# Kernel optimization log

Measured on AMD Instinct MI355X. Metric: run time of the kernel, lower is better.

Reference implementation:

```python
import jax, jax.numpy as jnp
import numpy as np


def _tridiag_solve(x, d, l, u):
    # Build dense tridiagonal M (faithful to the torch module) and solve.
    # x: [B, N, F]; d: [F]; l, u: [F-1]
    diag = jax.nn.softplus(d) + 2.0
    M = jnp.diag(diag) + jnp.diag(jnp.tanh(l), -1) + jnp.diag(jnp.tanh(u), 1)
    # solve M @ Y = x^T  -> Y: [B, F, N], then transpose back
    y = jnp.linalg.solve(M, jnp.swapaxes(x, -2, -1))
    return jnp.swapaxes(y, -2, -1)


def setup_inputs() -> dict:
    key = jax.random.key(0)
    ks = jax.random.split(key, 11)
    B, N = 8, 4096
    IN, HID, OUT = 512, 2048, 512
    s = 0.02
    return {
        "x": jax.random.normal(ks[0], (B, N, IN), dtype=jnp.float32),
        "d1": jax.random.normal(ks[1], (IN,), dtype=jnp.float32) * s,
        "l1": jax.random.normal(ks[2], (IN - 1,), dtype=jnp.float32) * s,
        "u1": jax.random.normal(ks[3], (IN - 1,), dtype=jnp.float32) * s,
        "W1": jax.random.normal(ks[4], (HID, IN), dtype=jnp.float32) * s,
        "b1": jax.random.normal(ks[5], (HID,), dtype=jnp.float32) * s,
        "d2": jax.random.normal(ks[6], (HID,), dtype=jnp.float32) * s,
        "l2": jax.random.normal(ks[7], (HID - 1,), dtype=jnp.float32) * s,
        "u2": jax.random.normal(ks[8], (HID - 1,), dtype=jnp.float32) * s,
        "W2": jax.random.normal(ks[9], (OUT, HID), dtype=jnp.float32) * s,
        "b2": jax.random.normal(ks[10], (OUT,), dtype=jnp.float32) * s,
    }


def reference(x, d1, l1, u1, W1, b1, d2, l2, u2, W2, b2):
    h = _tridiag_solve(x, d1, l1, u1)
    h = jax.nn.relu(jnp.einsum("bnf,hf->bnh", h, W1) + b1)
    h = _tridiag_solve(h, d2, l2, u2)
    out = jnp.einsum("bnh,oh->bno", h, W2) + b2
    return out
```

## Files before the change

### kernel.cpp

```cpp
#include <hip/hip_runtime.h>
#include <cstdint>

#define R_ROWS 32768
#define F1 512
#define F2 2048
#define NOUT 512

typedef __bf16 bf16x8 __attribute__((ext_vector_type(8)));
typedef float f32x4 __attribute__((ext_vector_type(4)));

__device__ __forceinline__ float bf2f(uint16_t b) {
  union { uint32_t u; float f; } v; v.u = ((uint32_t)b) << 16; return v.f;
}
__device__ __forceinline__ uint16_t f2bf(float f) {
  union { float f; uint32_t u; } v; v.f = f;
  uint32_t u = v.u;
  return (uint16_t)((u + 0x7fffu + ((u >> 16) & 1u)) >> 16);
}

union U4 { uint4 v; uint16_t s[8]; };

__global__ void sniff_kernel(const uint16_t* x, int* flag) {
  if (threadIdx.x == 0) {
    int bad = 0;
    for (int i = 0; i < 64; ++i) {
      uint32_t e = (x[i] >> 7) & 0xFFu;
      if (e != 0u && (e < 90u || e > 141u)) bad++;
    }
    *flag = (bad >= 8) ? 1 : 0;
  }
}

__global__ void conv_xb(const float* x, const float* b1, const float* b2,
                        uint16_t* xb, uint16_t* b1b, uint16_t* b2b,
                        const int* flag) {
  if (*flag != 1) return;
  const int NX = R_ROWS * F1 / 4;
  int q = blockIdx.x * blockDim.x + threadIdx.x;
  const float* src; uint16_t* dst; int base;
  if (q < NX)                        { src = x;  dst = xb;  base = q; }
  else if (q < NX + F2 / 4)          { src = b1; dst = b1b; base = q - NX; }
  else if (q < NX + F2/4 + NOUT/4)   { src = b2; dst = b2b; base = q - NX - F2/4; }
  else return;
  float4 v = ((const float4*)src)[base];
  ushort4 o;
  o.x = f2bf(v.x); o.y = f2bf(v.y); o.z = f2bf(v.z); o.w = f2bf(v.w);
  ((ushort4*)dst)[base] = o;
}

__launch_bounds__(256)
__global__ void prep_fused(const void* d1, const void* l1, const void* u1,
                           const void* d2, const void* l2, const void* u2,
                           float* f1, float* f2, const int* flag) {
  const bool inf32 = (*flag == 1);
  const int F = blockIdx.x ? F2 : F1;
  float* base = blockIdx.x ? f2 : f1;
  const void* dp = blockIdx.x ? d2 : d1;
  const void* lp = blockIdx.x ? l2 : l1;
  const void* up = blockIdx.x ? u2 : u1;

  __shared__ float sdiag[F2], stl[F2], stu[F2];

  for (int i = threadIdx.x; i < F; i += 256) {
    float dv = inf32 ? ((const float*)dp)[i] : bf2f(((const uint16_t*)dp)[i]);
    sdiag[i] = log1pf(expf(dv)) + 2.0f;
    bool in = i < F - 1;
    float lv = in ? (inf32 ? ((const float*)lp)[i] : bf2f(((const uint16_t*)lp)[i])) : 0.0f;
    float uv = in ? (inf32 ? ((const float*)up)[i] : bf2f(((const uint16_t*)up)[i])) : 0.0f;
    stl[i] = in ? tanhf(lv) : 0.0f;
    stu[i] = in ? tanhf(uv) : 0.0f;
  }
  __syncthreads();

  const int t  = threadIdx.x;
  const int CH = F >> 8;
  const int s0 = t * CH;
  const int j0 = (s0 >= 16) ? (s0 - 16) : 0;
  float b  = sdiag[j0];
  float ib = __builtin_amdgcn_rcpf(b);
  for (int j = j0 + 1; j < s0; ++j) {
    b  = fmaf(-stu[j - 1] * stl[j - 1], ib, sdiag[j]);
    ib = __builtin_amdgcn_rcpf(b);
  }
  #pragma unroll
  for (int q = 0; q < 8; ++q) {
    if (q >= CH) break;
    int i = s0 + q;
    float w, nb;
    if (i == 0) { w = 0.0f; nb = sdiag[0]; }
    else        { w = stu[i - 1] * ib; nb = fmaf(-w, stl[i - 1], sdiag[i]); }
    ib = __builtin_amdgcn_rcpf(nb);
    base[3 * F + i] = w;
    base[4 * F + i] = ib;
    base[5 * F + i] = stl[i] * ib;
  }
}

template<int F>
__launch_bounds__(256)
__global__ void solve_fused(const void* X, uint16_t* Y, const float* fact,
                            const int* flag, int allow_f32) {
  const bool inf32 = allow_f32 && (*flag == 1);
  constexpr int LPR = F / 32;
  constexpr int FP = F + (F >> 5);
  __shared__ float sfw[FP], sib[FP], sbk[FP];
  __shared__ uint4 sout[1024];
  for (int i = threadIdx.x; i < F; i += 256) {
    int ii = i + (i >> 5);
    sfw[ii] = fact[3 * F + i];
    sib[ii] = fact[4 * F + i];
    sbk[ii] = fact[5 * F + i];
  }
  __syncthreads();
  const int tid = threadIdx.x;
  int gt  = blockIdx.x * 256 + tid;
  int row = gt / LPR;
  int j   = gt % LPR;
  int k0  = j * 32;
  const size_t rb = (size_t)row * F;

  float xc[32];
  if (inf32) {
    const float* xr = (const float*)X + rb + k0;
    #pragma unroll
    for (int t = 0; t < 8; ++t) {
      float4 v = ((const float4*)xr)[t];
      xc[4*t] = v.x; xc[4*t+1] = v.y; xc[4*t+2] = v.z; xc[4*t+3] = v.w;
    }
  } else {
    const uint16_t* xr = (const uint16_t*)X + rb + k0;
    #pragma unroll
    for (int t = 0; t < 4; ++t) {
      U4 in; in.v = ((const uint4*)xr)[t];
      #pragma unroll
      for (int s = 0; s < 8; ++s) xc[8*t+s] = bf2f(in.s[s]);
    }
  }

  float dp = 0.0f;
  if (j > 0) {
    float xw[16];
    if (inf32) {
      const float* xr = (const float*)X + rb + k0 - 16;
      #pragma unroll
      for (int t = 0; t < 4; ++t) {
        float4 v = ((const float4*)xr)[t];
        xw[4*t] = v.x; xw[4*t+1] = v.y; xw[4*t+2] = v.z; xw[4*t+3] = v.w;
      }
    } else {
      const uint16_t* xr = (const uint16_t*)X + rb + k0 - 16;
      #pragma unroll
      for (int t = 0; t < 2; ++t) {
        U4 in; in.v = ((const uint4*)xr)[t];
        #pragma unroll
        for (int s = 0; s < 8; ++s) xw[8*t+s] = bf2f(in.s[s]);
      }
    }
    #pragma unroll
    for (int t = 0; t < 16; ++t) {
      int k = k0 - 16 + t;
      dp = fmaf(-sfw[k + (k >> 5)], dp, xw[t]);
    }
  }
  float dpv[32];
  #pragma unroll
  for (int t = 0; t < 32; ++t) {
    int k = k0 + t;
    dp = fmaf(-sfw[k + (k >> 5)], dp, xc[t]);
    dpv[t] = dp;
  }

  float wdp[16];
  #pragma unroll
  for (int t = 0; t < 16; ++t) wdp[t] = __shfl_down(dpv[t], 1);
  float yn = 0.0f;
  if (j < LPR - 1) {
    #pragma unroll
    for (int t = 15; t >= 0; --t) {
      int k = k0 + 32 + t;
      int kk = k + (k >> 5);
      yn = fmaf(-sbk[kk], yn, wdp[t] * sib[kk]);
    }
  }
  U4 out[4];
  #pragma unroll
  for (int t = 31; t >= 0; --t) {
    int k = k0 + t;
    int kk = k + (k >> 5);
    yn = fmaf(-sbk[kk], yn, dpv[t] * sib[kk]);
    out[t >> 3].s[t & 7] = f2bf(yn);
  }
  #pragma unroll
  for (int t = 0; t < 4; ++t) sout[tid * 4 + t] = out[t].v;
  __syncthreads();
  uint4* yg = (uint4*)Y + (size_t)blockIdx.x * 1024;
  #pragma unroll
  for (int i = 0; i < 4; ++i) yg[i * 256 + tid] = sout[i * 256 + tid];
}

__device__ __forceinline__ void gl_lds16(const uint16_t* g, uint16_t* l) {
  __builtin_amdgcn_global_load_lds((const __attribute__((address_space(1))) void*)g,
                                   (__attribute__((address_space(3))) void*)l, 16, 0, 0);
}

#define LOFF(bb, ab, h) ((bb) * 32768 + (ab) * 16384 + (h) * 8192)

#define GSTG(gp, bb, ab, h, kt) do {                                              \
    gl_lds16((gp) + (size_t)(h) * 128 * K + (kt),        lds + LOFF(bb, ab, h) + w * 512);        \
    gl_lds16((gp) + ((size_t)(h) * 128 + 64) * K + (kt), lds + LOFF(bb, ab, h) + 4096 + w * 512); \
  } while (0)

#define RD_A(mq) do {                                                             \
    _Pragma("unroll")                                                             \
    for (int fi = 0; fi < 4; ++fi) {                                              \
      af[fi][0] = *(const bf16x8*)(lds + curA + (mq) * 8192 + arow + fi * 1024 + c0); \
      af[fi][1] = *(const bf16x8*)(lds + curA + (mq) * 8192 + arow + fi * 1024 + c1); \
    }                                                                             \
  } while (0)

#define RD_B(nq) do {                                                             \
    _Pragma("unroll")                                                             \
    for (int fj = 0; fj < 2; ++fj) {                                              \
      bfr[nq][fj][0] = *(const bf16x8*)(lds + curB + (nq) * 8192 + brow + fj * 1024 + c0); \
      bfr[nq][fj][1] = *(const bf16x8*)(lds + curB + (nq) * 8192 + brow + fj * 1024 + c1); \
    }                                                                             \
  } while (0)

#define MMA_QUAD(mq, nq) do {                                                     \
    _Pragma("unroll")                                                             \
    for (int fi = 0; fi < 4; ++fi) {                                              \
      _Pragma("unroll")                                                           \
      for (int fj = 0; fj < 2; ++fj) {                                            \
        acc[(mq)*4+fi][(nq)*2+fj] = __builtin_amdgcn_mfma_f32_16x16x32_bf16(      \
            af[fi][0], bfr[nq][fj][0], acc[(mq)*4+fi][(nq)*2+fj], 0, 0, 0);       \
        acc[(mq)*4+fi][(nq)*2+fj] = __builtin_amdgcn_mfma_f32_16x16x32_bf16(      \
            af[fi][1], bfr[nq][fj][1], acc[(mq)*4+fi][(nq)*2+fj], 0, 0, 0);       \
      }                                                                           \
    }                                                                             \
  } while (0)

#define VMC(n) asm volatile("s_waitcnt vmcnt(" #n ")" ::: "memory")
#define BAR()  __builtin_amdgcn_s_barrier()
#define LGK0() do { asm volatile("s_waitcnt lgkmcnt(0)" ::: "memory");            \
                    __builtin_amdgcn_sched_barrier(0); } while (0)

template<bool RELU, bool FINAL, int NTN>
__launch_bounds__(512, 2)
__global__ void gemm8(const uint16_t* __restrict__ Aa, const uint16_t* __restrict__ Ab,
                      const uint16_t* __restrict__ Bw,
                      const uint16_t* __restrict__ bias0, const uint16_t* __restrict__ bias1,
                      void* __restrict__ Cout, int Nn, int K, const int* flag) {
  __shared__ __align__(16) uint16_t lds[65536];
  const int f = *flag;
  const uint16_t* A    = f ? Ab : Aa;
  const uint16_t* bias = f ? bias1 : bias0;

  const int tid = threadIdx.x;
  const int w = tid >> 6;
  const int l = tid & 63;
  const int wm = w >> 2;
  const int wn = w & 3;

  const int b = blockIdx.x;
  const int x = b & 7;
  const int g = b >> 3;
  const int nb = g & (NTN - 1);
  const int mb = (g / NTN) * 8 + x;
  const int MB = mb * 256, NB = nb * 256;
  const int NT = K >> 6;

  const int srow = w * 8 + (l >> 3);
  const int sch  = (l & 7) ^ ((l >> 3) & 7);
  const uint16_t* ag = A  + (size_t)(MB + srow) * K + sch * 8;
  const uint16_t* bg = Bw + (size_t)(NB + srow) * K + sch * 8;

  const int c0 = (((l >> 4) ^ (l & 7)) << 3);
  const int c1 = c0 ^ 32;
  const int arow = (wm * 64 + (l & 15)) * 64;
  const int brow = (wn * 32 + (l & 15)) * 64;

  f32x4 acc[8][4] = {};
  bf16x8 af[4][2];
  bf16x8 bfr[2][2][2];

  GSTG(ag, 0, 0, 0, 0);
  GSTG(bg, 0, 1, 0, 0);
  GSTG(bg, 0, 1, 1, 0);
  GSTG(ag, 0, 0, 1, 0);
  VMC(4);
  BAR();

  for (int t = 0; t < NT - 1; ++t) {
    const int cur  = t & 1;
    const int nxt  = cur ^ 1;
    const int curA = cur * 32768;
    const int curB = curA + 16384;
    const int kn   = (t + 1) * 64;
    RD_A(0); RD_B(0);
    GSTG(ag, nxt, 0, 0, kn);
    VMC(4); BAR(); LGK0();
    __builtin_amdgcn_s_setprio(1); MMA_QUAD(0, 0); __builtin_amdgcn_s_setprio(0);
    BAR();
    RD_B(1);
    GSTG(bg, nxt, 1, 0, kn);
    VMC(4); BAR(); LGK0();
    __builtin_amdgcn_s_setprio(1); MMA_QUAD(0, 1); __builtin_amdgcn_s_setprio(0);
    BAR();
    RD_A(1);
    GSTG(bg, nxt, 1, 1, kn);
    BAR(); LGK0();
    __builtin_amdgcn_s_setprio(1); MMA_QUAD(1, 0); __builtin_amdgcn_s_setprio(0);
    BAR();
    GSTG(ag, nxt, 0, 1, kn);
    VMC(4); BAR();
    __builtin_amdgcn_s_setprio(1); MMA_QUAD(1, 1); __builtin_amdgcn_s_setprio(0);
    BAR();
  }

  {
    const int curA = ((NT - 1) & 1) * 32768;
    const int curB = curA + 16384;
    RD_A(0); RD_B(0);
    __builtin_amdgcn_s_setprio(1); MMA_QUAD(0, 0); __builtin_amdgcn_s_setprio(0);
    VMC(2); BAR();
    RD_B(1);
    __builtin_amdgcn_s_setprio(1); MMA_QUAD(0, 1); __builtin_amdgcn_s_setprio(0);
    VMC(0); BAR();
    RD_A(1);
    MMA_QUAD(1, 0);
    MMA_QUAD(1, 1);
  }

  const bool outf32 = FINAL && (f != 0);
  const int ccol  = l & 15;
  const int crow4 = (l >> 4) * 4;
  #pragma unroll
  for (int j = 0; j < 4; ++j) {
    int gcol = NB + (j >> 1) * 128 + wn * 32 + (j & 1) * 16 + ccol;
    float bv = bf2f(bias[gcol]);
    #pragma unroll
    for (int i = 0; i < 8; ++i) {
      int grow = MB + (i >> 2) * 128 + wm * 64 + (i & 3) * 16 + crow4;
      #pragma unroll
      for (int rr = 0; rr < 4; ++rr) {
        float v = acc[i][j][rr] + bv;
        if (RELU) v = fmaxf(v, 0.0f);
        size_t idx = (size_t)(grow + rr) * Nn + gcol;
        if (outf32) ((float*)Cout)[idx]    = v;
        else        ((uint16_t*)Cout)[idx] = f2bf(v);
      }
    }
  }
}

extern "C" void kernel_launch(void* const* d_in, const int* in_sizes, int n_in,
                              void* d_out, int out_size, void* d_ws, size_t ws_size,
                              hipStream_t stream) {
  const void* x  = d_in[0];
  const void* d1 = d_in[1];
  const void* l1 = d_in[2];
  const void* u1 = d_in[3];
  const void* W1 = d_in[4];
  const void* b1 = d_in[5];
  const void* d2 = d_in[6];
  const void* l2 = d_in[7];
  const void* u2 = d_in[8];
  const void* W2 = d_in[9];
  const void* b2 = d_in[10];

  char* ws = (char*)d_ws;
  int*      flag = (int*)ws;
  float*    f1   = (float*)(ws + 256);
  float*    f2   = (float*)(ws + (64 << 10));
  uint16_t* b1b  = (uint16_t*)(ws + (128 << 10));
  uint16_t* b2b  = (uint16_t*)(ws + (136 << 10));
  uint16_t* W1s  = (uint16_t*)(ws + (1 << 20));
  uint16_t* W2s  = (uint16_t*)(ws + (3 << 20));
  uint16_t* xb   = (uint16_t*)(ws + ((size_t)8 << 20));
  uint16_t* H1   = (uint16_t*)(ws + ((size_t)40 << 20));

  sniff_kernel<<<1, 64, 0, stream>>>((const uint16_t*)x, flag);

  prep_fused<<<2, 256, 0, stream>>>(d1, l1, u1, d2, l2, u2, f1, f2, flag);

  solve_fused<F1><<<128, 256, 0, stream>>>(W1, W1s, f1, flag, 1);
  solve_fused<F2><<<128, 256, 0, stream>>>(W2, W2s, f2, flag, 1);

  {
    int quads = R_ROWS * F1 / 4 + F2 / 4 + NOUT / 4;
    conv_xb<<<(quads + 255) / 256, 256, 0, stream>>>(
        (const float*)x, (const float*)b1, (const float*)b2, xb, b1b, b2b, flag);
  }

  gemm8<true, false, 8><<<1024, 512, 0, stream>>>(
      (const uint16_t*)x, xb, W1s, (const uint16_t*)b1, b1b, H1, F2, F1, flag);

  gemm8<false, true, 2><<<256, 512, 0, stream>>>(
      H1, H1, W2s, (const uint16_t*)b2, b2b, d_out, NOUT, F2, flag);
}
```

Baseline: 319.2 us.

## Fuse preprocessing launches and cut barriers in the GEMM main loop

Folds the input-dtype sniff and bias conversion into the prep kernel. It also merges both weight tridiagonal solves and the x-to-bf16 conversion into one launch by splitting the work on block index. This removes three kernel launches and their serialization gaps. Separately, the GEMM main loop is rescheduled to issue more LDS fragment reads up front and wait on partial lgkmcnt counts, dropping from eight barriers per K-step to two. This raises register pressure and makes correctness depend on the hand-tuned waitcnt values.

```diff
diff --git a/kernel.cpp b/kernel.cpp
--- a/kernel.cpp
+++ b/kernel.cpp
@@ -20,39 +20,25 @@
 
 union U4 { uint4 v; uint16_t s[8]; };
 
-__global__ void sniff_kernel(const uint16_t* x, int* flag) {
-  if (threadIdx.x == 0) {
-    int bad = 0;
-    for (int i = 0; i < 64; ++i) {
-      uint32_t e = (x[i] >> 7) & 0xFFu;
-      if (e != 0u && (e < 90u || e > 141u)) bad++;
-    }
-    *flag = (bad >= 8) ? 1 : 0;
-  }
-}
-
-__global__ void conv_xb(const float* x, const float* b1, const float* b2,
-                        uint16_t* xb, uint16_t* b1b, uint16_t* b2b,
-                        const int* flag) {
-  if (*flag != 1) return;
-  const int NX = R_ROWS * F1 / 4;
-  int q = blockIdx.x * blockDim.x + threadIdx.x;
-  const float* src; uint16_t* dst; int base;
-  if (q < NX)                        { src = x;  dst = xb;  base = q; }
-  else if (q < NX + F2 / 4)          { src = b1; dst = b1b; base = q - NX; }
-  else if (q < NX + F2/4 + NOUT/4)   { src = b2; dst = b2b; base = q - NX - F2/4; }
-  else return;
-  float4 v = ((const float4*)src)[base];
-  ushort4 o;
-  o.x = f2bf(v.x); o.y = f2bf(v.y); o.z = f2bf(v.z); o.w = f2bf(v.w);
-  ((ushort4*)dst)[base] = o;
+__device__ __forceinline__ int sniff_x(const uint16_t* x) {
+  int bad = 0;
+  #pragma unroll 8
+  for (int i = 0; i < 64; ++i) {
+    uint32_t e = (x[i] >> 7) & 0xFFu;
+    if (e != 0u && (e < 90u || e > 141u)) bad++;
+  }
+  return (bad >= 8) ? 1 : 0;
 }
 
 __launch_bounds__(256)
-__global__ void prep_fused(const void* d1, const void* l1, const void* u1,
+__global__ void prep_fused(const void* x,
+                           const void* d1, const void* l1, const void* u1,
                            const void* d2, const void* l2, const void* u2,
-                           float* f1, float* f2, const int* flag) {
-  const bool inf32 = (*flag == 1);
+                           const void* b1, const void* b2,
+                           float* f1, float* f2,
+                           uint16_t* b1b, uint16_t* b2b, int* flag) {
+  const bool inf32 = sniff_x((const uint16_t*)x) != 0;
+  if (blockIdx.x == 0 && threadIdx.x == 0) *flag = inf32 ? 1 : 0;
   const int F = blockIdx.x ? F2 : F1;
   float* base = blockIdx.x ? f2 : f1;
   const void* dp = blockIdx.x ? d2 : d1;
@@ -69,6 +55,12 @@
     float uv = in ? (inf32 ? ((const float*)up)[i] : bf2f(((const uint16_t*)up)[i])) : 0.0f;
     stl[i] = in ? tanhf(lv) : 0.0f;
     stu[i] = in ? tanhf(uv) : 0.0f;
+  }
+  if (inf32) {
+    const float* bsrc = blockIdx.x ? (const float*)b1 : (const float*)b2;
+    uint16_t*    bdst = blockIdx.x ? b1b : b2b;
+    const int    bn   = blockIdx.x ? F2 : NOUT;
+    for (int i = threadIdx.x; i < bn; i += 256) bdst[i] = f2bf(bsrc[i]);
   }
   __syncthreads();
 
@@ -97,14 +89,10 @@
 }
 
 template<int F>
-__launch_bounds__(256)
-__global__ void solve_fused(const void* X, uint16_t* Y, const float* fact,
-                            const int* flag, int allow_f32) {
-  const bool inf32 = allow_f32 && (*flag == 1);
+__device__ void solve_rows(const void* X, uint16_t* Y, const float* fact,
+                           bool inf32, int blk,
+                           float* sfw, float* sib, float* sbk, uint4* sout) {
   constexpr int LPR = F / 32;
-  constexpr int FP = F + (F >> 5);
-  __shared__ float sfw[FP], sib[FP], sbk[FP];
-  __shared__ uint4 sout[1024];
   for (int i = threadIdx.x; i < F; i += 256) {
     int ii = i + (i >> 5);
     sfw[ii] = fact[3 * F + i];
@@ -113,7 +101,7 @@
   }
   __syncthreads();
   const int tid = threadIdx.x;
-  int gt  = blockIdx.x * 256 + tid;
+  int gt  = blk * 256 + tid;
   int row = gt / LPR;
   int j   = gt % LPR;
   int k0  = j * 32;
@@ -193,9 +181,31 @@
   #pragma unroll
   for (int t = 0; t < 4; ++t) sout[tid * 4 + t] = out[t].v;
   __syncthreads();
-  uint4* yg = (uint4*)Y + (size_t)blockIdx.x * 1024;
+  uint4* yg = (uint4*)Y + (size_t)blk * 1024;
   #pragma unroll
   for (int i = 0; i < 4; ++i) yg[i * 256 + tid] = sout[i * 256 + tid];
+}
+
+#define FP2 (F2 + (F2 >> 5))
+__launch_bounds__(256)
+__global__ void mid_fused(const void* x, const void* W1, const void* W2,
+                          uint16_t* W1s, uint16_t* W2s, uint16_t* xb,
+                          const float* f1, const float* f2, const int* flag) {
+  __shared__ float sfw[FP2], sib[FP2], sbk[FP2];
+  __shared__ uint4 sout[1024];
+  const bool inf32 = (*flag == 1);
+  const int b = blockIdx.x;
+  if (b < 128) {
+    solve_rows<F1>(W1, W1s, f1, inf32, b, sfw, sib, sbk, sout);
+  } else if (b < 256) {
+    solve_rows<F2>(W2, W2s, f2, inf32, b - 128, sfw, sib, sbk, sout);
+  } else if (inf32) {
+    int q = (b - 256) * 256 + threadIdx.x;
+    float4 v = ((const float4*)x)[q];
+    ushort4 o;
+    o.x = f2bf(v.x); o.y = f2bf(v.y); o.z = f2bf(v.z); o.w = f2bf(v.w);
+    ((ushort4*)xb)[q] = o;
+  }
 }
 
 __device__ __forceinline__ void gl_lds16(const uint16_t* g, uint16_t* l) {
@@ -210,19 +220,19 @@
     gl_lds16((gp) + ((size_t)(h) * 128 + 64) * K + (kt), lds + LOFF(bb, ab, h) + 4096 + w * 512); \
   } while (0)
 
-#define RD_A(mq) do {                                                             \
+#define RD_A(ba, mq) do {                                                         \
     _Pragma("unroll")                                                             \
     for (int fi = 0; fi < 4; ++fi) {                                              \
-      af[fi][0] = *(const bf16x8*)(lds + curA + (mq) * 8192 + arow + fi * 1024 + c0); \
-      af[fi][1] = *(const bf16x8*)(lds + curA + (mq) * 8192 + arow + fi * 1024 + c1); \
+      af[fi][0] = *(const bf16x8*)(lds + (ba) + (mq) * 8192 + arow + fi * 1024 + c0); \
+      af[fi][1] = *(const bf16x8*)(lds + (ba) + (mq) * 8192 + arow + fi * 1024 + c1); \
     }                                                                             \
   } while (0)
 
-#define RD_B(nq) do {                                                             \
+#define RD_B(ba, nq) do {                                                         \
     _Pragma("unroll")                                                             \
     for (int fj = 0; fj < 2; ++fj) {                                              \
-      bfr[nq][fj][0] = *(const bf16x8*)(lds + curB + (nq) * 8192 + brow + fj * 1024 + c0); \
-      bfr[nq][fj][1] = *(const bf16x8*)(lds + curB + (nq) * 8192 + brow + fj * 1024 + c1); \
+      bfr[nq][fj][0] = *(const bf16x8*)(lds + (ba) + (nq) * 8192 + brow + fj * 1024 + c0); \
+      bfr[nq][fj][1] = *(const bf16x8*)(lds + (ba) + (nq) * 8192 + brow + fj * 1024 + c1); \
     }                                                                             \
   } while (0)
 
@@ -241,8 +251,11 @@
 
 #define VMC(n) asm volatile("s_waitcnt vmcnt(" #n ")" ::: "memory")
 #define BAR()  __builtin_amdgcn_s_barrier()
-#define LGK0() do { asm volatile("s_waitcnt lgkmcnt(0)" ::: "memory");            \
-                    __builtin_amdgcn_sched_barrier(0); } while (0)
+#define SB0()  __builtin_amdgcn_sched_barrier(0)
+#define LGKC(n) do { asm volatile("s_waitcnt lgkmcnt(" #n ")" ::: "memory");      \
+                     __builtin_amdgcn_sched_barrier(0); } while (0)
+#define P1() __builtin_amdgcn_s_setprio(1)
+#define P0() __builtin_amdgcn_s_setprio(0)
 
 template<bool RELU, bool FINAL, int NTN>
 __launch_bounds__(512, 2)
@@ -287,8 +300,7 @@
   GSTG(bg, 0, 1, 0, 0);
   GSTG(bg, 0, 1, 1, 0);
   GSTG(ag, 0, 0, 1, 0);
-  VMC(4);
-  BAR();
+  VMC(2); BAR();
 
   for (int t = 0; t < NT - 1; ++t) {
     const int cur  = t & 1;
@@ -296,39 +308,32 @@
     const int curA = cur * 32768;
     const int curB = curA + 16384;
     const int kn   = (t + 1) * 64;
-    RD_A(0); RD_B(0);
+
+    RD_A(curA, 0); RD_B(curB, 0); RD_B(curB, 1);
+    SB0();
     GSTG(ag, nxt, 0, 0, kn);
-    VMC(4); BAR(); LGK0();
-    __builtin_amdgcn_s_setprio(1); MMA_QUAD(0, 0); __builtin_amdgcn_s_setprio(0);
-    BAR();
-    RD_B(1);
     GSTG(bg, nxt, 1, 0, kn);
-    VMC(4); BAR(); LGK0();
-    __builtin_amdgcn_s_setprio(1); MMA_QUAD(0, 1); __builtin_amdgcn_s_setprio(0);
-    BAR();
-    RD_A(1);
+    LGKC(4);  P1(); MMA_QUAD(0, 0); P0();
+    LGKC(0);  P1(); MMA_QUAD(0, 1); P0();
+    VMC(4); BAR();
+    RD_A(curA, 1);
+    SB0();
     GSTG(bg, nxt, 1, 1, kn);
-    BAR(); LGK0();
-    __builtin_amdgcn_s_setprio(1); MMA_QUAD(1, 0); __builtin_amdgcn_s_setprio(0);
-    BAR();
     GSTG(ag, nxt, 0, 1, kn);
-    VMC(4); BAR();
-    __builtin_amdgcn_s_setprio(1); MMA_QUAD(1, 1); __builtin_amdgcn_s_setprio(0);
-    BAR();
+    LGKC(0);  P1(); MMA_QUAD(1, 0); MMA_QUAD(1, 1); P0();
+    VMC(2); BAR();
   }
 
   {
     const int curA = ((NT - 1) & 1) * 32768;
     const int curB = curA + 16384;
-    RD_A(0); RD_B(0);
-    __builtin_amdgcn_s_setprio(1); MMA_QUAD(0, 0); __builtin_amdgcn_s_setprio(0);
-    VMC(2); BAR();
-    RD_B(1);
-    __builtin_amdgcn_s_setprio(1); MMA_QUAD(0, 1); __builtin_amdgcn_s_setprio(0);
+    RD_A(curA, 0); RD_B(curB, 0); RD_B(curB, 1);
+    SB0();
+    LGKC(4);  P1(); MMA_QUAD(0, 0); P0();
+    LGKC(0);  P1(); MMA_QUAD(0, 1); P0();
     VMC(0); BAR();
-    RD_A(1);
-    MMA_QUAD(1, 0);
-    MMA_QUAD(1, 1);
+    RD_A(curA, 1);
+    LGKC(0);  P1(); MMA_QUAD(1, 0); MMA_QUAD(1, 1); P0();
   }
 
   const bool outf32 = FINAL && (f != 0);
@@ -379,18 +384,11 @@
   uint16_t* xb   = (uint16_t*)(ws + ((size_t)8 << 20));
   uint16_t* H1   = (uint16_t*)(ws + ((size_t)40 << 20));
 
-  sniff_kernel<<<1, 64, 0, stream>>>((const uint16_t*)x, flag);
-
-  prep_fused<<<2, 256, 0, stream>>>(d1, l1, u1, d2, l2, u2, f1, f2, flag);
-
-  solve_fused<F1><<<128, 256, 0, stream>>>(W1, W1s, f1, flag, 1);
-  solve_fused<F2><<<128, 256, 0, stream>>>(W2, W2s, f2, flag, 1);
-
-  {
-    int quads = R_ROWS * F1 / 4 + F2 / 4 + NOUT / 4;
-    conv_xb<<<(quads + 255) / 256, 256, 0, stream>>>(
-        (const float*)x, (const float*)b1, (const float*)b2, xb, b1b, b2b, flag);
-  }
+  prep_fused<<<2, 256, 0, stream>>>(x, d1, l1, u1, d2, l2, u2, b1, b2,
+                                    f1, f2, b1b, b2b, flag);
+
+  mid_fused<<<256 + (R_ROWS * F1 / 4) / 256, 256, 0, stream>>>(
+      x, W1, W2, W1s, W2s, xb, f1, f2, flag);
 
   gemm8<true, false, 8><<<1024, 512, 0, stream>>>(
       (const uint16_t*)x, xb, W1s, (const uint16_t*)b1, b1b, H1, F2, F1, flag);
```

Result: faster. 309.1 us (-3.2%).
